# Kernel tuning notes

Hardware: AMD Instinct MI355X
Metric: run time of the kernel (lower is better)

The kernel has to match this reference:

```python
import jax, jax.numpy as jnp
import numpy as np

EPS = 1e-15
PROJ_EPS = 1e-5
N_NODES = 100000

def _norm(x):
    return jnp.maximum(jnp.sqrt(jnp.sum(x * x, axis=-1, keepdims=True)), EPS)

def _tanh(x):
    return jnp.tanh(jnp.clip(x, -15.0, 15.0))

def _atanh(x):
    return jnp.arctanh(jnp.clip(x, -1.0 + 1e-7, 1.0 - 1e-7))

def log_map_zero(y):
    n = _norm(y)
    return (_atanh(n) / n) * y

def exp_map_zero(v):
    n = _norm(v)
    return (_tanh(n) / n) * v

def hyperbolic_projection(x):
    # clip norm to 1 - PROJ_EPS (stay inside the Poincare ball)
    n = _norm(x)
    scale = jnp.minimum(jnp.float32(1.0), (1.0 - PROJ_EPS) / n)
    return x * scale

def mobius_addition(x, y):
    x2 = jnp.sum(x * x, axis=-1, keepdims=True)
    y2 = jnp.sum(y * y, axis=-1, keepdims=True)
    xy = jnp.sum(x * y, axis=-1, keepdims=True)
    num = (1.0 + 2.0 * xy + y2) * x + (1.0 - x2) * y
    den = 1.0 + 2.0 * xy + x2 * y2
    return num / jnp.maximum(den, EPS)

def setup_inputs() -> dict:
    key = jax.random.key(0)
    k0, k1, k2, k3, k4, k5 = jax.random.split(key, 6)
    N, E, D_IN, D_OUT = N_NODES, 640000, 128, 128
    # entity embeddings: points inside the Poincare ball
    x = jax.random.normal(k0, (N, D_IN), dtype=jnp.float32) * 0.01
    x = hyperbolic_projection(x)
    # xavier-uniform weight
    a = np.sqrt(6.0 / (D_IN + D_OUT)).astype(np.float32)
    W = jax.random.uniform(k1, (D_IN, D_OUT), minval=-a, maxval=a, dtype=jnp.float32)
    bias = jax.random.normal(k2, (1, D_OUT), dtype=jnp.float32) * 0.01
    adj_row = jax.random.randint(k3, (E,), 0, N, dtype=jnp.int32)
    adj_col = jax.random.randint(k4, (E,), 0, N, dtype=jnp.int32)
    adj_val = jax.random.uniform(k5, (E,), dtype=jnp.float32) * 0.125
    return {"ents_embed_input": x, "W_ent": W, "bias_vec": bias,
            "adj_val": adj_val, "adj_row": adj_row, "adj_col": adj_col}

def reference(ents_embed_input, W_ent, bias_vec, adj_val, adj_row, adj_col):
    # log map to tangent space at origin, then dense linear map
    tangent = log_map_zero(ents_embed_input)                 # [N, D_in]
    mapped = tangent @ W_ent                                 # [N, D_out]
    # sparse adjacency aggregation: out[i] = sum_e val[e] * mapped[col[e]], row[e] == i
    msgs = adj_val[:, None] * mapped[adj_col]                # [E, D_out]
    agg = jax.ops.segment_sum(msgs, adj_row, num_segments=N_NODES)
    h = hyperbolic_projection(exp_map_zero(agg))
    # mobius bias addition
    b = hyperbolic_projection(exp_map_zero(bias_vec))
    out = hyperbolic_projection(mobius_addition(h, b))
    return out
```

## Files before the change

kernel.cpp:

```cpp
#include <hip/hip_runtime.h>
#include <hip/hip_bf16.h>

#define D 128
#define FEPS 1e-15f
#define PROJ_EPS 1e-5f

typedef __attribute__((ext_vector_type(8))) short short8v;
typedef __attribute__((ext_vector_type(4))) float f32x4;

__device__ __forceinline__ unsigned pack_bf16x2(float lo, float hi) {
    __hip_bfloat16 h0 = __float2bfloat16(lo);
    __hip_bfloat16 h1 = __float2bfloat16(hi);
    unsigned u0 = *reinterpret_cast<unsigned short*>(&h0);
    unsigned u1 = *reinterpret_cast<unsigned short*>(&h1);
    return u0 | (u1 << 16);
}

__device__ __forceinline__ float bf_lo(unsigned u) { return __uint_as_float(u << 16); }
__device__ __forceinline__ float bf_hi(unsigned u) { return __uint_as_float(u & 0xffff0000u); }

__device__ __forceinline__ float fast_tanh_clamped(float n) {
    float nc = fminf(n, 15.f);
    float e2 = __expf(2.f * nc);
    return 1.f - __fdividef(2.f, e2 + 1.f);
}

__global__ __launch_bounds__(512) void k_hist(const int* __restrict__ rowi,
                                              int* __restrict__ cnt, int E) {
    int e = blockIdx.x * 512 + threadIdx.x;
    if (e < E) atomicAdd(&cnt[rowi[e]], 1);
}

__global__ __launch_bounds__(256) void k_scan1(const int* __restrict__ cnt,
                                               int* __restrict__ ex,
                                               int* __restrict__ bsum, int Nn) {
    __shared__ int ts[256];
    int t = threadIdx.x, b = blockIdx.x;
    int base = b * 1024 + t * 4;
    int v0 = (base + 0 < Nn) ? cnt[base + 0] : 0;
    int v1 = (base + 1 < Nn) ? cnt[base + 1] : 0;
    int v2 = (base + 2 < Nn) ? cnt[base + 2] : 0;
    int v3 = (base + 3 < Nn) ? cnt[base + 3] : 0;
    int s = v0 + v1 + v2 + v3;
    ts[t] = s;
    __syncthreads();
    for (int off = 1; off < 256; off <<= 1) {
        int add = (t >= off) ? ts[t - off] : 0;
        __syncthreads();
        ts[t] += add;
        __syncthreads();
    }
    int excl = ts[t] - s;
    if (t == 255) bsum[b] = ts[t];
    if (base + 0 < Nn) ex[base + 0] = excl;
    if (base + 1 < Nn) ex[base + 1] = excl + v0;
    if (base + 2 < Nn) ex[base + 2] = excl + v0 + v1;
    if (base + 3 < Nn) ex[base + 3] = excl + v0 + v1 + v2;
}

__global__ void k_scan2(const int* __restrict__ bsum, int* __restrict__ bsumx, int nb) {
    __shared__ int ts[128];
    int t = threadIdx.x;
    int v = (t < nb) ? bsum[t] : 0;
    ts[t] = v;
    __syncthreads();
    for (int off = 1; off < 128; off <<= 1) {
        int add = (t >= off) ? ts[t - off] : 0;
        __syncthreads();
        ts[t] += add;
        __syncthreads();
    }
    bsumx[t] = ts[t] - v;
}

__global__ __launch_bounds__(256) void k_scan3(int* __restrict__ rowptr,
                                               const int* __restrict__ bsumx,
                                               int* __restrict__ cursor, int Nn, int E) {
    int i = blockIdx.x * 256 + threadIdx.x;
    if (i < Nn) {
        int v = rowptr[i] + bsumx[i >> 10];
        rowptr[i] = v;
        cursor[i] = v;
    }
    if (i == 0) rowptr[Nn] = E;
}

__global__ __launch_bounds__(512) void k_gemm_scatter(
    const float* __restrict__ x, const float* __restrict__ W,
    __hip_bfloat16* __restrict__ mapped, int Nn, int NT, int GBg, int SBs,
    const int* __restrict__ rowi, const int* __restrict__ coli,
    const float* __restrict__ val, int* __restrict__ cursor,
    int2* __restrict__ sedge, int E)
{
    __shared__ uint4 lsW4[2048];
    __shared__ uint4 lsC4[2048];

    const int tid = threadIdx.x;

    if (blockIdx.x >= GBg) {
        int stride = SBs * 512;
        for (int e = (blockIdx.x - GBg) * 512 + tid; e < E; e += stride) {
            int cv = coli[e];
            float vv = val[e];
            int p = atomicAdd(&cursor[rowi[e]], 1);
            sedge[p] = make_int2(cv, __float_as_int(vv));
        }
        return;
    }

    const int w = tid >> 6, l = tid & 63;
    const int q = l & 15, khi = l >> 4;

#pragma unroll
    for (int it = 0; it < 4; ++it) {
        int i = it * 512 + tid;
        int col = i & 127, kg = i >> 7;
        unsigned p0 = pack_bf16x2(W[(kg * 8 + 0) * D + col], W[(kg * 8 + 1) * D + col]);
        unsigned p1 = pack_bf16x2(W[(kg * 8 + 2) * D + col], W[(kg * 8 + 3) * D + col]);
        unsigned p2 = pack_bf16x2(W[(kg * 8 + 4) * D + col], W[(kg * 8 + 5) * D + col]);
        unsigned p3 = pack_bf16x2(W[(kg * 8 + 6) * D + col], W[(kg * 8 + 7) * D + col]);
        lsW4[col * 16 + (kg ^ (col & 15))] = make_uint4(p0, p1, p2, p3);
    }
    __syncthreads();

    const short8v* lsB = (const short8v*)lsW4;
    unsigned* lsc = (unsigned*)lsC4;
    const int cbase = w * 1024;

#pragma unroll 1
    for (int tt = blockIdx.x; tt < NT; tt += GBg) {
        const int rowbase = tt * 128;
        const int row = rowbase + w * 16 + q;
        const bool rv = row < Nn;
        const float* xr = x + (size_t)row * D;
        float4 xa[8];
        float nn = 0.f;
#pragma unroll
        for (int ks = 0; ks < 4; ++ks) {
            float4 p0 = make_float4(0.f, 0.f, 0.f, 0.f), p1 = p0;
            if (rv) {
                p0 = *reinterpret_cast<const float4*>(xr + ks * 32 + khi * 8);
                p1 = *reinterpret_cast<const float4*>(xr + ks * 32 + khi * 8 + 4);
            }
            xa[2 * ks] = p0; xa[2 * ks + 1] = p1;
            nn += p0.x * p0.x + p0.y * p0.y + p0.z * p0.z + p0.w * p0.w
                + p1.x * p1.x + p1.y * p1.y + p1.z * p1.z + p1.w * p1.w;
        }
        nn += __shfl_xor(nn, 16, 64);
        nn += __shfl_xor(nn, 32, 64);
        float n = fmaxf(sqrtf(nn), FEPS);
        float c = fminf(n, 1.f - 1e-7f);
        float s = __fdividef(0.5f * __logf(__fdividef(1.f + c, 1.f - c)), n);

        union { unsigned u[4]; short8v v; } af[4];
#pragma unroll
        for (int ks = 0; ks < 4; ++ks) {
            float4 p0 = xa[2 * ks], p1 = xa[2 * ks + 1];
            af[ks].u[0] = pack_bf16x2(s * p0.x, s * p0.y);
            af[ks].u[1] = pack_bf16x2(s * p0.z, s * p0.w);
            af[ks].u[2] = pack_bf16x2(s * p1.x, s * p1.y);
            af[ks].u[3] = pack_bf16x2(s * p1.z, s * p1.w);
        }

        f32x4 acc[8];
#pragma unroll
        for (int t = 0; t < 8; ++t) acc[t] = (f32x4){0.f, 0.f, 0.f, 0.f};

#pragma unroll
        for (int ks = 0; ks < 4; ++ks) {
#pragma unroll
            for (int t = 0; t < 8; ++t) {
                short8v b = lsB[(t * 16 + q) * 16 + ((ks * 4 + khi) ^ q)];
                acc[t] = __builtin_amdgcn_mfma_f32_16x16x32_bf16(af[ks].v, b, acc[t], 0, 0, 0);
            }
        }

#pragma unroll
        for (int t = 0; t < 8; ++t) {
#pragma unroll
            for (int r = 0; r < 4; ++r) {
                float self = acc[t][r];
                float other = __shfl_xor(self, 1, 64);
                unsigned pw = (q & 1) ? pack_bf16x2(other, self) : pack_bf16x2(self, other);
                int rl = khi * 4 + r;
                int cp = t * 8 + (q >> 1);
                lsc[cbase + rl * 64 + (cp ^ (khi << 3))] = pw;
            }
        }
#pragma unroll
        for (int i4 = 0; i4 < 4; ++i4) {
            int rl = i4 * 4 + (l >> 4);
            int ro = rowbase + w * 16 + rl;
            int cp4 = (l & 15) * 4;
            uint4 vv = lsC4[(cbase + rl * 64 + (cp4 ^ (i4 << 3))) >> 2];
            if (ro < Nn)
                *reinterpret_cast<uint4*>(mapped + (size_t)ro * D + (l & 15) * 8) = vv;
        }
    }
}

__global__ __launch_bounds__(256) void k_aggfin(
    const uint4* __restrict__ mapped4, const int2* __restrict__ sedge,
    const int* __restrict__ rowptr, const float* __restrict__ bias,
    float* __restrict__ out, int Nn)
{
    const int tid = threadIdx.x;
    const int w = tid >> 6, l = tid & 63;
    const int g = l >> 4, q = l & 15;
    const int row = blockIdx.x * 16 + w * 4 + g;

    float4 rb0 = *reinterpret_cast<const float4*>(bias + q * 8);
    float4 rb1 = *reinterpret_cast<const float4*>(bias + q * 8 + 4);
    float bn2 = rb0.x * rb0.x + rb0.y * rb0.y + rb0.z * rb0.z + rb0.w * rb0.w
              + rb1.x * rb1.x + rb1.y * rb1.y + rb1.z * rb1.z + rb1.w * rb1.w;
#pragma unroll
    for (int o = 8; o > 0; o >>= 1) bn2 += __shfl_xor(bn2, o, 64);
    float bn = fmaxf(sqrtf(bn2), FEPS);
    float bt = fast_tanh_clamped(bn);
    float bs = __fdividef(bt, bn);
    float ben2 = bs * bs * bn2;
    float bpn = fmaxf(sqrtf(ben2), FEPS);
    float bps = fminf(1.f, __fdividef(1.f - PROJ_EPS, bpn));
    float bsc = bs * bps;
    float y2 = bps * bps * ben2;
    float bj[8] = { rb0.x * bsc, rb0.y * bsc, rb0.z * bsc, rb0.w * bsc,
                    rb1.x * bsc, rb1.y * bsc, rb1.z * bsc, rb1.w * bsc };

    if (row >= Nn) return;
    int beg = rowptr[row], end = rowptr[row + 1];

    float acc[8] = {0.f, 0.f, 0.f, 0.f, 0.f, 0.f, 0.f, 0.f};
    int e = beg;
    for (; e + 3 < end; e += 4) {
        int2 d0 = sedge[e], d1 = sedge[e + 1], d2 = sedge[e + 2], d3 = sedge[e + 3];
        uint4 u0 = mapped4[(size_t)d0.x * 16 + q];
        uint4 u1 = mapped4[(size_t)d1.x * 16 + q];
        uint4 u2 = mapped4[(size_t)d2.x * 16 + q];
        uint4 u3 = mapped4[(size_t)d3.x * 16 + q];
        float v0 = __int_as_float(d0.y), v1 = __int_as_float(d1.y);
        float v2 = __int_as_float(d2.y), v3 = __int_as_float(d3.y);
        acc[0] += v0 * bf_lo(u0.x); acc[1] += v0 * bf_hi(u0.x);
        acc[2] += v0 * bf_lo(u0.y); acc[3] += v0 * bf_hi(u0.y);
        acc[4] += v0 * bf_lo(u0.z); acc[5] += v0 * bf_hi(u0.z);
        acc[6] += v0 * bf_lo(u0.w); acc[7] += v0 * bf_hi(u0.w);
        acc[0] += v1 * bf_lo(u1.x); acc[1] += v1 * bf_hi(u1.x);
        acc[2] += v1 * bf_lo(u1.y); acc[3] += v1 * bf_hi(u1.y);
        acc[4] += v1 * bf_lo(u1.z); acc[5] += v1 * bf_hi(u1.z);
        acc[6] += v1 * bf_lo(u1.w); acc[7] += v1 * bf_hi(u1.w);
        acc[0] += v2 * bf_lo(u2.x); acc[1] += v2 * bf_hi(u2.x);
        acc[2] += v2 * bf_lo(u2.y); acc[3] += v2 * bf_hi(u2.y);
        acc[4] += v2 * bf_lo(u2.z); acc[5] += v2 * bf_hi(u2.z);
        acc[6] += v2 * bf_lo(u2.w); acc[7] += v2 * bf_hi(u2.w);
        acc[0] += v3 * bf_lo(u3.x); acc[1] += v3 * bf_hi(u3.x);
        acc[2] += v3 * bf_lo(u3.y); acc[3] += v3 * bf_hi(u3.y);
        acc[4] += v3 * bf_lo(u3.z); acc[5] += v3 * bf_hi(u3.z);
        acc[6] += v3 * bf_lo(u3.w); acc[7] += v3 * bf_hi(u3.w);
    }
    for (; e < end; ++e) {
        int2 d0 = sedge[e];
        uint4 u0 = mapped4[(size_t)d0.x * 16 + q];
        float v0 = __int_as_float(d0.y);
        acc[0] += v0 * bf_lo(u0.x); acc[1] += v0 * bf_hi(u0.x);
        acc[2] += v0 * bf_lo(u0.y); acc[3] += v0 * bf_hi(u0.y);
        acc[4] += v0 * bf_lo(u0.z); acc[5] += v0 * bf_hi(u0.z);
        acc[6] += v0 * bf_lo(u0.w); acc[7] += v0 * bf_hi(u0.w);
    }

    float n2 = 0.f, ab = 0.f;
#pragma unroll
    for (int j = 0; j < 8; ++j) { n2 += acc[j] * acc[j]; ab += acc[j] * bj[j]; }
#pragma unroll
    for (int o = 8; o > 0; o >>= 1) {
        n2 += __shfl_xor(n2, o, 64);
        ab += __shfl_xor(ab, o, 64);
    }

    float n = fmaxf(sqrtf(n2), FEPS);
    float t = fast_tanh_clamped(n);
    float s = __fdividef(t, n);
    float en2 = s * s * n2;
    float pn = fmaxf(sqrtf(en2), FEPS);
    float ps = fminf(1.f, __fdividef(1.f - PROJ_EPS, pn));
    float hs = s * ps;
    float x2 = ps * ps * en2;

    float xy = hs * ab;
    float cA = 1.f + 2.f * xy + y2;
    float cB = 1.f - x2;
    float den = fmaxf(1.f + 2.f * xy + x2 * y2, FEPS);
    float inv = __fdividef(1.f, den);
    float zn2 = inv * inv * (cA * cA * x2 + 2.f * cA * cB * xy + cB * cB * y2);
    float zn = fmaxf(sqrtf(zn2), FEPS);
    float zs = fminf(1.f, __fdividef(1.f - PROJ_EPS, zn));
    float f = inv * zs;
    float chs = cA * hs * f, cBf = cB * f;

    float4 o0 = make_float4(chs * acc[0] + cBf * bj[0], chs * acc[1] + cBf * bj[1],
                            chs * acc[2] + cBf * bj[2], chs * acc[3] + cBf * bj[3]);
    float4 o1 = make_float4(chs * acc[4] + cBf * bj[4], chs * acc[5] + cBf * bj[5],
                            chs * acc[6] + cBf * bj[6], chs * acc[7] + cBf * bj[7]);
    *reinterpret_cast<float4*>(out + (size_t)row * D + q * 8) = o0;
    *reinterpret_cast<float4*>(out + (size_t)row * D + q * 8 + 4) = o1;
}

extern "C" void kernel_launch(void* const* d_in, const int* in_sizes, int n_in,
                              void* d_out, int out_size, void* d_ws, size_t ws_size,
                              hipStream_t stream) {
    const float* x    = (const float*)d_in[0];
    const float* W    = (const float*)d_in[1];
    const float* bias = (const float*)d_in[2];
    const float* val  = (const float*)d_in[3];
    const int*   rowi = (const int*)d_in[4];
    const int*   coli = (const int*)d_in[5];
    const int N = in_sizes[0] / D;
    const int E = in_sizes[3];

    char* ws = (char*)d_ws;
    int*   cnt    = (int*)ws;
    int*   rowptr = (int*)(ws + 400000);
    int*   bsum   = (int*)(ws + 800512);
    int*   bsumx  = (int*)(ws + 801024);
    int*   cursor = (int*)(ws + 801536);
    int2*  sedge  = (int2*)(ws + 1201536);
    __hip_bfloat16* mapped = (__hip_bfloat16*)(ws + 1201536 + (size_t)E * 8);
    float* out = (float*)d_out;

    hipMemsetAsync(cnt, 0, (size_t)N * sizeof(int), stream);
    k_hist<<<(E + 511) / 512, 512, 0, stream>>>(rowi, cnt, E);

    int nb = (N + 1023) / 1024;
    k_scan1<<<nb, 256, 0, stream>>>(cnt, rowptr, bsum, N);
    k_scan2<<<1, 128, 0, stream>>>(bsum, bsumx, nb);
    k_scan3<<<(N + 255) / 256, 256, 0, stream>>>(rowptr, bsumx, cursor, N, E);

    const int NT  = (N + 127) / 128;
    const int GBg = 384;
    const int SBs = 128;
    k_gemm_scatter<<<GBg + SBs, 512, 0, stream>>>(x, W, mapped, N, NT, GBg, SBs,
                                                  rowi, coli, val, cursor, sedge, E);

    k_aggfin<<<(N + 15) / 16, 256, 0, stream>>>((const uint4*)mapped,
                                                (const int2*)sedge, rowptr,
                                                bias, out, N);
}
```

Measured before the change: 128.2 us.

## Split CSR build into eight edge-group sub-buckets to reduce atomic contention

The histogram, scan and scatter now keep eight per-group counters per row, one per contiguous edge chunk group, and scan a group-major 8N array. Each scatter block only touches one group's cursors. The aggregation kernel reads sixteen boundaries per row via shuffles and walks up to eight sub-ranges. This is meant to reduce atomic contention, but it makes the scan eight times larger and adds branching in the gather loop.

```diff
diff --git a/kernel.cpp b/kernel.cpp
--- a/kernel.cpp
+++ b/kernel.cpp
@@ -25,22 +25,26 @@
     return 1.f - __fdividef(2.f, e2 + 1.f);
 }
 
-__global__ __launch_bounds__(512) void k_hist(const int* __restrict__ rowi,
-                                              int* __restrict__ cnt, int E) {
+__global__ __launch_bounds__(512) void k_hist8(const int* __restrict__ rowi,
+                                               int* __restrict__ cnt8,
+                                               int E, int Nn, int Eper) {
     int e = blockIdx.x * 512 + threadIdx.x;
-    if (e < E) atomicAdd(&cnt[rowi[e]], 1);
+    if (e < E) {
+        int g = e / Eper;
+        atomicAdd(&cnt8[(size_t)g * Nn + rowi[e]], 1);
+    }
 }
 
 __global__ __launch_bounds__(256) void k_scan1(const int* __restrict__ cnt,
                                                int* __restrict__ ex,
-                                               int* __restrict__ bsum, int Nn) {
+                                               int* __restrict__ bsum, int Ntot) {
     __shared__ int ts[256];
     int t = threadIdx.x, b = blockIdx.x;
     int base = b * 1024 + t * 4;
-    int v0 = (base + 0 < Nn) ? cnt[base + 0] : 0;
-    int v1 = (base + 1 < Nn) ? cnt[base + 1] : 0;
-    int v2 = (base + 2 < Nn) ? cnt[base + 2] : 0;
-    int v3 = (base + 3 < Nn) ? cnt[base + 3] : 0;
+    int v0 = (base + 0 < Ntot) ? cnt[base + 0] : 0;
+    int v1 = (base + 1 < Ntot) ? cnt[base + 1] : 0;
+    int v2 = (base + 2 < Ntot) ? cnt[base + 2] : 0;
+    int v3 = (base + 3 < Ntot) ? cnt[base + 3] : 0;
     int s = v0 + v1 + v2 + v3;
     ts[t] = s;
     __syncthreads();
@@ -52,19 +56,20 @@
     }
     int excl = ts[t] - s;
     if (t == 255) bsum[b] = ts[t];
-    if (base + 0 < Nn) ex[base + 0] = excl;
-    if (base + 1 < Nn) ex[base + 1] = excl + v0;
-    if (base + 2 < Nn) ex[base + 2] = excl + v0 + v1;
-    if (base + 3 < Nn) ex[base + 3] = excl + v0 + v1 + v2;
-}
-
-__global__ void k_scan2(const int* __restrict__ bsum, int* __restrict__ bsumx, int nb) {
-    __shared__ int ts[128];
+    if (base + 0 < Ntot) ex[base + 0] = excl;
+    if (base + 1 < Ntot) ex[base + 1] = excl + v0;
+    if (base + 2 < Ntot) ex[base + 2] = excl + v0 + v1;
+    if (base + 3 < Ntot) ex[base + 3] = excl + v0 + v1 + v2;
+}
+
+__global__ __launch_bounds__(1024) void k_scan2(const int* __restrict__ bsum,
+                                                int* __restrict__ bsumx, int nb) {
+    __shared__ int ts[1024];
     int t = threadIdx.x;
     int v = (t < nb) ? bsum[t] : 0;
     ts[t] = v;
     __syncthreads();
-    for (int off = 1; off < 128; off <<= 1) {
+    for (int off = 1; off < 1024; off <<= 1) {
         int add = (t >= off) ? ts[t - off] : 0;
         __syncthreads();
         ts[t] += add;
@@ -73,23 +78,24 @@
     bsumx[t] = ts[t] - v;
 }
 
-__global__ __launch_bounds__(256) void k_scan3(int* __restrict__ rowptr,
+__global__ __launch_bounds__(256) void k_scan3(int* __restrict__ base8,
                                                const int* __restrict__ bsumx,
-                                               int* __restrict__ cursor, int Nn, int E) {
+                                               int* __restrict__ cursor8,
+                                               int Ntot, int E) {
     int i = blockIdx.x * 256 + threadIdx.x;
-    if (i < Nn) {
-        int v = rowptr[i] + bsumx[i >> 10];
-        rowptr[i] = v;
-        cursor[i] = v;
-    }
-    if (i == 0) rowptr[Nn] = E;
+    if (i < Ntot) {
+        int v = base8[i] + bsumx[i >> 10];
+        base8[i] = v;
+        cursor8[i] = v;
+    }
+    if (i == 0) base8[Ntot] = E;
 }
 
 __global__ __launch_bounds__(512) void k_gemm_scatter(
     const float* __restrict__ x, const float* __restrict__ W,
-    __hip_bfloat16* __restrict__ mapped, int Nn, int NT, int GBg, int SBs,
+    __hip_bfloat16* __restrict__ mapped, int Nn, int NT, int GBg,
     const int* __restrict__ rowi, const int* __restrict__ coli,
-    const float* __restrict__ val, int* __restrict__ cursor,
+    const float* __restrict__ val, int* __restrict__ cursor8,
     int2* __restrict__ sedge, int E)
 {
     __shared__ uint4 lsW4[2048];
@@ -98,11 +104,19 @@
     const int tid = threadIdx.x;
 
     if (blockIdx.x >= GBg) {
-        int stride = SBs * 512;
-        for (int e = (blockIdx.x - GBg) * 512 + tid; e < E; e += stride) {
+        const int j = blockIdx.x - GBg;
+        const int g = j & 7;
+        const int ib = j >> 3;
+        const int Echunk = (E + 127) >> 7;
+        const int chunk = g * 16 + ib;
+        int e0 = chunk * Echunk;
+        int e1 = min(e0 + Echunk, E);
+        int* cur = cursor8 + (size_t)g * Nn;
+        for (int e = e0 + tid; e < e1; e += 512) {
+            int r = rowi[e];
             int cv = coli[e];
             float vv = val[e];
-            int p = atomicAdd(&cursor[rowi[e]], 1);
+            int p = atomicAdd(&cur[r], 1);
             sedge[p] = make_int2(cv, __float_as_int(vv));
         }
         return;
@@ -199,9 +213,16 @@
     }
 }
 
+__device__ __forceinline__ void accum8(float* acc, uint4 u, float v) {
+    acc[0] += v * bf_lo(u.x); acc[1] += v * bf_hi(u.x);
+    acc[2] += v * bf_lo(u.y); acc[3] += v * bf_hi(u.y);
+    acc[4] += v * bf_lo(u.z); acc[5] += v * bf_hi(u.z);
+    acc[6] += v * bf_lo(u.w); acc[7] += v * bf_hi(u.w);
+}
+
 __global__ __launch_bounds__(256) void k_aggfin(
     const uint4* __restrict__ mapped4, const int2* __restrict__ sedge,
-    const int* __restrict__ rowptr, const float* __restrict__ bias,
+    const int* __restrict__ base8, const float* __restrict__ bias,
     float* __restrict__ out, int Nn)
 {
     const int tid = threadIdx.x;
@@ -227,43 +248,38 @@
                     rb1.x * bsc, rb1.y * bsc, rb1.z * bsc, rb1.w * bsc };
 
     if (row >= Nn) return;
-    int beg = rowptr[row], end = rowptr[row + 1];
+
+    int hdr = base8[(size_t)(q & 7) * Nn + row + (q >> 3)];
+    const int gl = l & 48;
+    int b[8], en_[8];
+#pragma unroll
+    for (int s2 = 0; s2 < 8; ++s2) {
+        b[s2]   = __shfl(hdr, gl + s2, 64);
+        en_[s2] = __shfl(hdr, gl + 8 + s2, 64);
+    }
 
     float acc[8] = {0.f, 0.f, 0.f, 0.f, 0.f, 0.f, 0.f, 0.f};
-    int e = beg;
-    for (; e + 3 < end; e += 4) {
-        int2 d0 = sedge[e], d1 = sedge[e + 1], d2 = sedge[e + 2], d3 = sedge[e + 3];
-        uint4 u0 = mapped4[(size_t)d0.x * 16 + q];
-        uint4 u1 = mapped4[(size_t)d1.x * 16 + q];
-        uint4 u2 = mapped4[(size_t)d2.x * 16 + q];
-        uint4 u3 = mapped4[(size_t)d3.x * 16 + q];
-        float v0 = __int_as_float(d0.y), v1 = __int_as_float(d1.y);
-        float v2 = __int_as_float(d2.y), v3 = __int_as_float(d3.y);
-        acc[0] += v0 * bf_lo(u0.x); acc[1] += v0 * bf_hi(u0.x);
-        acc[2] += v0 * bf_lo(u0.y); acc[3] += v0 * bf_hi(u0.y);
-        acc[4] += v0 * bf_lo(u0.z); acc[5] += v0 * bf_hi(u0.z);
-        acc[6] += v0 * bf_lo(u0.w); acc[7] += v0 * bf_hi(u0.w);
-        acc[0] += v1 * bf_lo(u1.x); acc[1] += v1 * bf_hi(u1.x);
-        acc[2] += v1 * bf_lo(u1.y); acc[3] += v1 * bf_hi(u1.y);
-        acc[4] += v1 * bf_lo(u1.z); acc[5] += v1 * bf_hi(u1.z);
-        acc[6] += v1 * bf_lo(u1.w); acc[7] += v1 * bf_hi(u1.w);
-        acc[0] += v2 * bf_lo(u2.x); acc[1] += v2 * bf_hi(u2.x);
-        acc[2] += v2 * bf_lo(u2.y); acc[3] += v2 * bf_hi(u2.y);
-        acc[4] += v2 * bf_lo(u2.z); acc[5] += v2 * bf_hi(u2.z);
-        acc[6] += v2 * bf_lo(u2.w); acc[7] += v2 * bf_hi(u2.w);
-        acc[0] += v3 * bf_lo(u3.x); acc[1] += v3 * bf_hi(u3.x);
-        acc[2] += v3 * bf_lo(u3.y); acc[3] += v3 * bf_hi(u3.y);
-        acc[4] += v3 * bf_lo(u3.z); acc[5] += v3 * bf_hi(u3.z);
-        acc[6] += v3 * bf_lo(u3.w); acc[7] += v3 * bf_hi(u3.w);
-    }
-    for (; e < end; ++e) {
-        int2 d0 = sedge[e];
-        uint4 u0 = mapped4[(size_t)d0.x * 16 + q];
-        float v0 = __int_as_float(d0.y);
-        acc[0] += v0 * bf_lo(u0.x); acc[1] += v0 * bf_hi(u0.x);
-        acc[2] += v0 * bf_lo(u0.y); acc[3] += v0 * bf_hi(u0.y);
-        acc[4] += v0 * bf_lo(u0.z); acc[5] += v0 * bf_hi(u0.z);
-        acc[6] += v0 * bf_lo(u0.w); acc[7] += v0 * bf_hi(u0.w);
+    while (true) {
+        int2 d[4]; bool h[4];
+#pragma unroll
+        for (int s = 0; s < 4; ++s) {
+            int p = -1;
+            if (b[s] < en_[s])            { p = b[s]; b[s] += 1; }
+            else if (b[s + 4] < en_[s + 4]) { p = b[s + 4]; b[s + 4] += 1; }
+            h[s] = (p >= 0);
+            if (h[s]) d[s] = sedge[p];
+        }
+        uint4 u[4];
+#pragma unroll
+        for (int s = 0; s < 4; ++s)
+            if (h[s]) u[s] = mapped4[(size_t)d[s].x * 16 + q];
+#pragma unroll
+        for (int s = 0; s < 4; ++s)
+            if (h[s]) accum8(acc, u[s], __int_as_float(d[s].y));
+        bool any = false;
+#pragma unroll
+        for (int s = 0; s < 8; ++s) any = any || (b[s] < en_[s]);
+        if (!any) break;
     }
 
     float n2 = 0.f, ab = 0.f;
@@ -314,32 +330,38 @@
     const int*   coli = (const int*)d_in[5];
     const int N = in_sizes[0] / D;
     const int E = in_sizes[3];
+    const int N8 = 8 * N;
 
     char* ws = (char*)d_ws;
-    int*   cnt    = (int*)ws;
-    int*   rowptr = (int*)(ws + 400000);
-    int*   bsum   = (int*)(ws + 800512);
-    int*   bsumx  = (int*)(ws + 801024);
-    int*   cursor = (int*)(ws + 801536);
-    int2*  sedge  = (int2*)(ws + 1201536);
-    __hip_bfloat16* mapped = (__hip_bfloat16*)(ws + 1201536 + (size_t)E * 8);
+    size_t off = 0;
+    int* cnt8 = (int*)(ws + off);      off += (size_t)N8 * 4;
+    int* base8 = (int*)(ws + off);     off += ((size_t)N8 + 1) * 4;
+    off = (off + 63) & ~(size_t)63;
+    int* bsum = (int*)(ws + off);      off += 1024 * 4;
+    int* bsumx = (int*)(ws + off);     off += 1024 * 4;
+    int* cursor8 = (int*)(ws + off);   off += (size_t)N8 * 4;
+    off = (off + 63) & ~(size_t)63;
+    int2* sedge = (int2*)(ws + off);   off += (size_t)E * 8;
+    __hip_bfloat16* mapped = (__hip_bfloat16*)(ws + off);
     float* out = (float*)d_out;
 
-    hipMemsetAsync(cnt, 0, (size_t)N * sizeof(int), stream);
-    k_hist<<<(E + 511) / 512, 512, 0, stream>>>(rowi, cnt, E);
-
-    int nb = (N + 1023) / 1024;
-    k_scan1<<<nb, 256, 0, stream>>>(cnt, rowptr, bsum, N);
-    k_scan2<<<1, 128, 0, stream>>>(bsum, bsumx, nb);
-    k_scan3<<<(N + 255) / 256, 256, 0, stream>>>(rowptr, bsumx, cursor, N, E);
+    const int Echunk = (E + 127) >> 7;
+    const int Eper = 16 * Echunk;
+
+    hipMemsetAsync(cnt8, 0, (size_t)N8 * sizeof(int), stream);
+    k_hist8<<<(E + 511) / 512, 512, 0, stream>>>(rowi, cnt8, E, N, Eper);
+
+    int nb = (N8 + 1023) / 1024;
+    k_scan1<<<nb, 256, 0, stream>>>(cnt8, base8, bsum, N8);
+    k_scan2<<<1, 1024, 0, stream>>>(bsum, bsumx, nb);
+    k_scan3<<<(N8 + 255) / 256, 256, 0, stream>>>(base8, bsumx, cursor8, N8, E);
 
     const int NT  = (N + 127) / 128;
     const int GBg = 384;
-    const int SBs = 128;
-    k_gemm_scatter<<<GBg + SBs, 512, 0, stream>>>(x, W, mapped, N, NT, GBg, SBs,
-                                                  rowi, coli, val, cursor, sedge, E);
+    k_gemm_scatter<<<GBg + 128, 512, 0, stream>>>(x, W, mapped, N, NT, GBg,
+                                                  rowi, coli, val, cursor8, sedge, E);
 
     k_aggfin<<<(N + 15) / 16, 256, 0, stream>>>((const uint4*)mapped,
-                                                (const int2*)sedge, rowptr,
+                                                (const int2*)sedge, base8,
                                                 bias, out, N);
 }
```

Result: slower. 149.7 us (+16.7%).
